# Optimization experiments

Hardware: AMD Instinct MI355X
Metric: run time of the kernel (lower is better)

The kernel has to match this reference:

```python
import jax, jax.numpy as jnp
import numpy as np

N, E = 50000, 800000
DIN, H, DOUT, L = 128, 128, 64, 3
NEG_SLOPE = 0.2  # PyG GATConv default


def setup_inputs() -> dict:
    key = jax.random.key(0)
    ks = jax.random.split(key, 12)
    s = lambda i, shape: (jax.random.normal(ks[i], shape, jnp.float32) * 0.05)
    return {
        "x": jax.random.normal(ks[0], (N, DIN), jnp.float32),
        "edge_index": jax.random.randint(ks[1], (2, E), 0, N, jnp.int64 if jax.config.jax_enable_x64 else jnp.int32),
        "W_emb": s(2, (DIN, H)), "b_emb": jnp.zeros((H,), jnp.float32),
        "gat_W": s(3, (L, H, H)), "gat_as": s(4, (L, H)), "gat_ad": s(5, (L, H)),
        "gat_b": jnp.zeros((L, H), jnp.float32),
        "Wn1": s(6, (H, H)), "bn1": jnp.zeros((H,), jnp.float32),
        "Wn2": s(7, (H, DOUT)), "bn2": jnp.zeros((DOUT,), jnp.float32),
        "We1": s(8, (2 * H, H)), "be1": jnp.zeros((H,), jnp.float32),
        "We2": s(9, (H, 3)), "be2": jnp.zeros((3,), jnp.float32),
    }


def _gat_layer(h, src, dst, n, W, a_src, a_dst, b):
    # Single-head GATConv (PyG defaults: heads=1, concat, self-loops already in src/dst)
    xw = h @ W                                   # [N, H]
    alpha_s = xw @ a_src                          # [N]
    alpha_d = xw @ a_dst                          # [N]
    logits = jax.nn.leaky_relu(alpha_s[src] + alpha_d[dst], NEG_SLOPE)  # [E']
    m = jax.ops.segment_max(logits, dst, num_segments=n)
    p = jnp.exp(logits - m[dst])
    denom = jax.ops.segment_sum(p, dst, num_segments=n)
    alpha = p / denom[dst]                        # softmax over incoming edges
    return jax.ops.segment_sum(alpha[:, None] * xw[src], dst, num_segments=n) + b


def reference(x, edge_index, W_emb, b_emb, gat_W, gat_as, gat_ad, gat_b,
              Wn1, bn1, Wn2, bn2, We1, be1, We2, be2):
    n = x.shape[0]
    src0, dst0 = edge_index[0], edge_index[1]
    loops = jnp.arange(n, dtype=src0.dtype)
    src = jnp.concatenate([src0, loops])          # GATConv adds self-loops by default
    dst = jnp.concatenate([dst0, loops])

    h = jax.nn.relu(x @ W_emb + b_emb)            # dropout off (eval mode)
    for l in range(L):
        h_new = _gat_layer(h, src, dst, n, gat_W[l], gat_as[l], gat_ad[l], gat_b[l])
        h = jax.nn.relu(h + h_new)                # residual + relu

    node_pred = jax.nn.relu(h @ Wn1 + bn1) @ Wn2 + bn2            # [N, DOUT]
    ef = jnp.concatenate([h[src0], h[dst0]], axis=1)              # vectorized edge gather [E, 2H]
    edge_pred = jax.nn.relu(ef @ We1 + be1) @ We2 + be2           # [E, 3]
    graph_emb = jnp.mean(h, axis=0, keepdims=True)                # batch=None path [1, H]
    return node_pred, edge_pred, graph_emb
```

## Files before the change

### kernel.cpp

```cpp
#include <hip/hip_runtime.h>

#define NNODES 50000
#define NEDGES 800000
#define HDIM 128
#define DOUT 64
#define NLAYERS 3
#define NEG_SLOPE 0.2f

#define NODE_OUT_ELEMS (NNODES * DOUT)
#define EDGE_OUT_ELEMS (NEDGES * 3)
#define GEMB_OFF (NODE_OUT_ELEMS + EDGE_OUT_ELEMS)

typedef __attribute__((ext_vector_type(8))) short short8;
typedef __attribute__((ext_vector_type(4))) float f32x4;
typedef unsigned long long u64;

__device__ __forceinline__ float bf2f(unsigned short u) {
    union { unsigned int i; float f; } v; v.i = ((unsigned int)u) << 16; return v.f;
}
__device__ __forceinline__ unsigned short f2bf(float f) {
    union { unsigned int i; float f; } v; v.f = f;
    unsigned int b = v.i;
    unsigned int r = (b + 0x7FFFu + ((b >> 16) & 1u)) >> 16;
    return (unsigned short)r;
}
__device__ __forceinline__ float leaky(float x) { return x > 0.f ? x : NEG_SLOPE * x; }
__device__ __forceinline__ float wread(const void* p, size_t i, int f32) {
    return f32 ? ((const float*)p)[i] : bf2f(((const unsigned short*)p)[i]);
}

__device__ __forceinline__ int eget(const int* e32, const int* iflag, int which, int e) {
    int idx = which * NEDGES + e;
    return (*iflag) ? e32[idx] : e32[2 * idx];
}

__global__ void init_kernel(int* cnt, int* cur, float* gsum, int* flags) {
    int i = blockIdx.x * 256 + threadIdx.x;
    if (i < NNODES) { cnt[i] = 0; cur[i] = 0; }
    if (blockIdx.x == 0) {
        if (threadIdx.x < HDIM) gsum[threadIdx.x] = 0.f;
        if (threadIdx.x < 2) flags[threadIdx.x] = 0;
    }
}

__global__ void detect_kernel(const unsigned short* xb, const int* e32,
                              int* fflag, int* iflag) {
    if (blockIdx.x == 0) {
        int hit = 0;
        for (int j = threadIdx.x; j < 4096; j += 256) {
            int e = (xb[j] >> 7) & 0xFF;
            if (e >= 0x90) hit = 1;
        }
        if (hit) atomicOr(fflag, 1);
    } else {
        int hit = 0;
        for (int t = threadIdx.x; t < 16384; t += 256) {
            int i = t * 48;
            if (e32[2 * i + 1] != 0) hit = 1;
        }
        if (__any(hit)) {
            if ((threadIdx.x & 63) == 0) atomicOr(iflag, 1);
        }
    }
}

__global__ void cvt_x_bf16_kernel(const void* x, unsigned short* xb,
                                  const int* f32flag) {
    int i = (blockIdx.x * 256 + threadIdx.x) * 4;
    if (*f32flag) {
        float4 v = *(const float4*)((const float*)x + i);
        unsigned short o[4] = {f2bf(v.x), f2bf(v.y), f2bf(v.z), f2bf(v.w)};
        *(uint2*)(xb + i) = *(uint2*)o;
    } else {
        *(uint2*)(xb + i) = *(const uint2*)((const unsigned short*)x + i);
    }
}

__global__ __launch_bounds__(256) void gemm_mfma_kernel(
    const unsigned short* __restrict__ A, const void* __restrict__ Bw,
    size_t b_off, const void* __restrict__ bias, unsigned short* __restrict__ C,
    int M, int relu, const int* __restrict__ f32flag)
{
    constexpr int KP = 128 + 8;
    __shared__ unsigned short sA[64 * KP];
    const int f32 = *f32flag;
    const int tid = threadIdx.x;
    const int row0 = blockIdx.x * 64;

    for (int c = tid; c < 64 * 16; c += 256) {
        int r = c >> 4, cp = c & 15;
        int gr = row0 + r;
        uint4 v = {0u, 0u, 0u, 0u};
        if (gr < M) v = *(const uint4*)(A + (size_t)gr * 128 + cp * 8);
        *(uint4*)(&sA[r * KP + cp * 8]) = v;
    }
    __syncthreads();

    const int wave = tid >> 6, lane = tid & 63;
    const int quad = lane >> 4, l15 = lane & 15;
    const int ncol0 = wave * 32;

    short8 bw[4][2];
    #pragma unroll
    for (int kk = 0; kk < 4; kk++)
        #pragma unroll
        for (int nt = 0; nt < 2; nt++) {
            int n = ncol0 + nt * 16 + l15;
            short8 t;
            #pragma unroll
            for (int j = 0; j < 8; j++)
                t[j] = (short)f2bf(wread(Bw, b_off + (size_t)(kk * 32 + quad * 8 + j) * 128 + n, f32));
            bw[kk][nt] = t;
        }

    float bv[2];
    #pragma unroll
    for (int nt = 0; nt < 2; nt++)
        bv[nt] = bias ? wread(bias, ncol0 + nt * 16 + l15, f32) : 0.f;

    f32x4 acc[4][2];
    #pragma unroll
    for (int mt = 0; mt < 4; mt++)
        #pragma unroll
        for (int nt = 0; nt < 2; nt++) {
            acc[mt][nt][0] = bv[nt]; acc[mt][nt][1] = bv[nt];
            acc[mt][nt][2] = bv[nt]; acc[mt][nt][3] = bv[nt];
        }

    #pragma unroll
    for (int kk = 0; kk < 4; kk++) {
        short8 a[4];
        #pragma unroll
        for (int mt = 0; mt < 4; mt++)
            a[mt] = *(const short8*)(&sA[(mt * 16 + l15) * KP + kk * 32 + quad * 8]);
        #pragma unroll
        for (int mt = 0; mt < 4; mt++)
            #pragma unroll
            for (int nt = 0; nt < 2; nt++)
                acc[mt][nt] = __builtin_amdgcn_mfma_f32_16x16x32_bf16(
                    a[mt], bw[kk][nt], acc[mt][nt], 0, 0, 0);
    }

    #pragma unroll
    for (int mt = 0; mt < 4; mt++)
        #pragma unroll
        for (int nt = 0; nt < 2; nt++)
            #pragma unroll
            for (int q = 0; q < 4; q++) {
                int row = row0 + mt * 16 + quad * 4 + q;
                if (row < M) {
                    float v = acc[mt][nt][q];
                    if (relu) v = fmaxf(v, 0.f);
                    C[(size_t)row * 128 + ncol0 + nt * 16 + l15] = f2bf(v);
                }
            }
}

__global__ __launch_bounds__(256) void node_mlp_kernel(
    const unsigned short* __restrict__ h, const void* __restrict__ Wn1,
    const void* __restrict__ bn1, const void* __restrict__ Wn2,
    const void* __restrict__ bn2, float* __restrict__ out, int M,
    const int* __restrict__ f32flag)
{
    constexpr int KP = 128 + 8;
    __shared__ unsigned short sA[64 * KP];
    const int f32 = *f32flag;
    const int tid = threadIdx.x;
    const int row0 = blockIdx.x * 64;

    for (int c = tid; c < 64 * 16; c += 256) {
        int r = c >> 4, cp = c & 15;
        int gr = row0 + r;
        uint4 v = {0u, 0u, 0u, 0u};
        if (gr < M) v = *(const uint4*)(h + (size_t)gr * 128 + cp * 8);
        *(uint4*)(&sA[r * KP + cp * 8]) = v;
    }
    __syncthreads();

    const int wave = tid >> 6, lane = tid & 63;
    const int quad = lane >> 4, l15 = lane & 15;
    const int ncol0 = wave * 32;

    {
        short8 bw[4][2];
        #pragma unroll
        for (int kk = 0; kk < 4; kk++)
            #pragma unroll
            for (int nt = 0; nt < 2; nt++) {
                int n = ncol0 + nt * 16 + l15;
                short8 t;
                #pragma unroll
                for (int j = 0; j < 8; j++)
                    t[j] = (short)f2bf(wread(Wn1, (size_t)(kk * 32 + quad * 8 + j) * 128 + n, f32));
                bw[kk][nt] = t;
            }
        float bv[2];
        #pragma unroll
        for (int nt = 0; nt < 2; nt++)
            bv[nt] = wread(bn1, ncol0 + nt * 16 + l15, f32);

        f32x4 acc[4][2];
        #pragma unroll
        for (int mt = 0; mt < 4; mt++)
            #pragma unroll
            for (int nt = 0; nt < 2; nt++) {
                acc[mt][nt][0] = bv[nt]; acc[mt][nt][1] = bv[nt];
                acc[mt][nt][2] = bv[nt]; acc[mt][nt][3] = bv[nt];
            }
        #pragma unroll
        for (int kk = 0; kk < 4; kk++) {
            short8 a[4];
            #pragma unroll
            for (int mt = 0; mt < 4; mt++)
                a[mt] = *(const short8*)(&sA[(mt * 16 + l15) * KP + kk * 32 + quad * 8]);
            #pragma unroll
            for (int mt = 0; mt < 4; mt++)
                #pragma unroll
                for (int nt = 0; nt < 2; nt++)
                    acc[mt][nt] = __builtin_amdgcn_mfma_f32_16x16x32_bf16(
                        a[mt], bw[kk][nt], acc[mt][nt], 0, 0, 0);
        }
        __syncthreads();
        #pragma unroll
        for (int mt = 0; mt < 4; mt++)
            #pragma unroll
            for (int nt = 0; nt < 2; nt++)
                #pragma unroll
                for (int q = 0; q < 4; q++) {
                    int r = mt * 16 + quad * 4 + q;
                    sA[r * KP + ncol0 + nt * 16 + l15] =
                        f2bf(fmaxf(acc[mt][nt][q], 0.f));
                }
        __syncthreads();
    }

    {
        const int col = wave * 16 + l15;
        short8 bw[4];
        #pragma unroll
        for (int kk = 0; kk < 4; kk++) {
            short8 t;
            #pragma unroll
            for (int j = 0; j < 8; j++)
                t[j] = (short)f2bf(wread(Wn2, (size_t)(kk * 32 + quad * 8 + j) * 64 + col, f32));
            bw[kk] = t;
        }
        float bv = wread(bn2, col, f32);
        f32x4 acc[4];
        #pragma unroll
        for (int mt = 0; mt < 4; mt++) {
            acc[mt][0] = bv; acc[mt][1] = bv; acc[mt][2] = bv; acc[mt][3] = bv;
        }
        #pragma unroll
        for (int kk = 0; kk < 4; kk++) {
            short8 a[4];
            #pragma unroll
            for (int mt = 0; mt < 4; mt++)
                a[mt] = *(const short8*)(&sA[(mt * 16 + l15) * KP + kk * 32 + quad * 8]);
            #pragma unroll
            for (int mt = 0; mt < 4; mt++)
                acc[mt] = __builtin_amdgcn_mfma_f32_16x16x32_bf16(
                    a[mt], bw[kk], acc[mt], 0, 0, 0);
        }
        #pragma unroll
        for (int mt = 0; mt < 4; mt++)
            #pragma unroll
            for (int q = 0; q < 4; q++) {
                int row = row0 + mt * 16 + quad * 4 + q;
                if (row < M) out[(size_t)row * 64 + col] = acc[mt][q];
            }
    }
}

__global__ __launch_bounds__(256) void edge_ab_kernel(
    const unsigned short* __restrict__ h, const void* __restrict__ We1,
    const void* __restrict__ be1, unsigned short* __restrict__ Axw,
    unsigned short* __restrict__ Bh, int M, const int* __restrict__ f32flag)
{
    constexpr int KP = 128 + 8;
    __shared__ unsigned short sA[64 * KP];
    const int f32 = *f32flag;
    const int tid = threadIdx.x;
    const int row0 = blockIdx.x * 64;

    for (int c = tid; c < 64 * 16; c += 256) {
        int r = c >> 4, cp = c & 15;
        int gr = row0 + r;
        uint4 v = {0u, 0u, 0u, 0u};
        if (gr < M) v = *(const uint4*)(h + (size_t)gr * 128 + cp * 8);
        *(uint4*)(&sA[r * KP + cp * 8]) = v;
    }
    __syncthreads();

    const int wave = tid >> 6, lane = tid & 63;
    const int quad = lane >> 4, l15 = lane & 15;
    const int ncol0 = wave * 32;

    #pragma unroll
    for (int half = 0; half < 2; half++) {
        const size_t b_off = (size_t)half * 128 * 128;
        unsigned short* Cp = half ? Bh : Axw;

        short8 bw[4][2];
        #pragma unroll
        for (int kk = 0; kk < 4; kk++)
            #pragma unroll
            for (int nt = 0; nt < 2; nt++) {
                int n = ncol0 + nt * 16 + l15;
                short8 t;
                #pragma unroll
                for (int j = 0; j < 8; j++)
                    t[j] = (short)f2bf(wread(We1, b_off + (size_t)(kk * 32 + quad * 8 + j) * 128 + n, f32));
                bw[kk][nt] = t;
            }
        float bv[2];
        #pragma unroll
        for (int nt = 0; nt < 2; nt++)
            bv[nt] = half ? 0.f : wread(be1, ncol0 + nt * 16 + l15, f32);

        f32x4 acc[4][2];
        #pragma unroll
        for (int mt = 0; mt < 4; mt++)
            #pragma unroll
            for (int nt = 0; nt < 2; nt++) {
                acc[mt][nt][0] = bv[nt]; acc[mt][nt][1] = bv[nt];
                acc[mt][nt][2] = bv[nt]; acc[mt][nt][3] = bv[nt];
            }
        #pragma unroll
        for (int kk = 0; kk < 4; kk++) {
            short8 a[4];
            #pragma unroll
            for (int mt = 0; mt < 4; mt++)
                a[mt] = *(const short8*)(&sA[(mt * 16 + l15) * KP + kk * 32 + quad * 8]);
            #pragma unroll
            for (int mt = 0; mt < 4; mt++)
                #pragma unroll
                for (int nt = 0; nt < 2; nt++)
                    acc[mt][nt] = __builtin_amdgcn_mfma_f32_16x16x32_bf16(
                        a[mt], bw[kk][nt], acc[mt][nt], 0, 0, 0);
        }
        #pragma unroll
        for (int mt = 0; mt < 4; mt++)
            #pragma unroll
            for (int nt = 0; nt < 2; nt++)
                #pragma unroll
                for (int q = 0; q < 4; q++) {
                    int row = row0 + mt * 16 + quad * 4 + q;
                    if (row < M)
                        Cp[(size_t)row * 128 + ncol0 + nt * 16 + l15] =
                            f2bf(acc[mt][nt][q]);
                }
    }
}

__global__ void alpha_kernel(const unsigned short* xw,
                             const void* gat_as, const void* gat_ad, int woff,
                             float* alpha_s, float* alpha_d,
                             const int* f32flag) {
    const int f32 = *f32flag;
    int wave = threadIdx.x >> 6, lane = threadIdx.x & 63;
    int n = blockIdx.x * 4 + wave;
    if (n >= NNODES) return;
    float v0 = bf2f(xw[(size_t)n * HDIM + lane]);
    float v1 = bf2f(xw[(size_t)n * HDIM + 64 + lane]);
    float ds = v0 * wread(gat_as, woff + lane, f32) + v1 * wread(gat_as, woff + 64 + lane, f32);
    float dd = v0 * wread(gat_ad, woff + lane, f32) + v1 * wread(gat_ad, woff + 64 + lane, f32);
    for (int d = 32; d >= 1; d >>= 1) { ds += __shfl_xor(ds, d); dd += __shfl_xor(dd, d); }
    if (lane == 0) { alpha_s[n] = ds; alpha_d[n] = dd; }
}

__global__ void count_kernel(const int* e32, const int* iflag, int* cnt) {
    int e = blockIdx.x * 256 + threadIdx.x;
    if (e < NEDGES) atomicAdd(&cnt[eget(e32, iflag, 1, e)], 1);
}
__global__ void scan1_kernel(const int* cnt, int* off, int* bsum) {
    __shared__ int s[256];
    int t = threadIdx.x, i = blockIdx.x * 256 + t;
    int v = (i < NNODES) ? cnt[i] : 0;
    s[t] = v;
    __syncthreads();
    for (int d = 1; d < 256; d <<= 1) {
        int add = (t >= d) ? s[t - d] : 0;
        __syncthreads();
        s[t] += add;
        __syncthreads();
    }
    if (i < NNODES) off[i] = s[t] - v;
    if (t == 255) bsum[blockIdx.x] = s[255];
}
__global__ void scan2_kernel(int* bsum, int nblk) {
    if (threadIdx.x == 0 && blockIdx.x == 0) {
        int run = 0;
        for (int c = 0; c < nblk; c++) { int t = bsum[c]; bsum[c] = run; run += t; }
    }
}
__global__ void scan3_kernel(int* off, const int* bsum) {
    int i = blockIdx.x * 256 + threadIdx.x;
    if (i < NNODES) off[i] += bsum[blockIdx.x];
}
__global__ void fill_kernel(const int* e32, const int* iflag, const int* off,
                            int* cur, u64* csrp, int use_pack) {
    int e = blockIdx.x * 256 + threadIdx.x;
    if (e < NEDGES) {
        int s = eget(e32, iflag, 0, e);
        int d = eget(e32, iflag, 1, e);
        int p = atomicAdd(&cur[d], 1);
        int pos = off[d] + p;
        if (use_pack)
            csrp[pos] = (u64)s | ((u64)d << 17) | ((u64)e << 34);
        else
            ((int*)csrp)[pos] = s;
    }
}

__global__ void aggregate_kernel(const unsigned short* __restrict__ xw,
                                 const float* __restrict__ as_, const float* __restrict__ ad_,
                                 const int* __restrict__ off, const u64* __restrict__ csrp,
                                 int use_pack, const void* __restrict__ gat_b, int boff,
                                 unsigned short* __restrict__ h,
                                 const int* __restrict__ f32flag) {
    const int f32 = *f32flag;
    int wave = threadIdx.x >> 6, lane = threadIdx.x & 63;
    int n = blockIdx.x * 4 + wave;
    if (n >= NNODES) return;
    int o0 = off[n];
    int o1 = (n == NNODES - 1) ? NEDGES : off[n + 1];
    int deg = o1 - o0;
    float adn = ad_[n];
    float lself = leaky(as_[n] + adn);

    int deg64 = deg < 64 ? deg : 64;
    int idxv = 0; float av = 0.f;
    if (lane < deg64) {
        idxv = use_pack ? (int)(csrp[o0 + lane] & 0x1FFFF)
                        : ((const int*)csrp)[o0 + lane];
        av = as_[idxv];
    }

    float m = lself;
    if (lane < deg64) m = fmaxf(m, leaky(av + adn));
    for (int i = 64 + lane; i < deg; i += 64) {
        int s = use_pack ? (int)(csrp[o0 + i] & 0x1FFFF)
                         : ((const int*)csrp)[o0 + i];
        m = fmaxf(m, leaky(as_[s] + adn));
    }
    #pragma unroll
    for (int d = 32; d >= 1; d >>= 1) m = fmaxf(m, __shfl_xor(m, d));

    const int slot = lane >> 4;
    const int l15  = lane & 15;
    float denom = 0.f;
    float acc[8];
    #pragma unroll
    for (int k = 0; k < 8; k++) acc[k] = 0.f;

    for (int t0 = 0; t0 < deg64; t0 += 4) {
        int i = t0 + slot;
        int sidx   = __shfl(idxv, i);
        float aval = __shfl(av, i);
        if (i < deg64) {
            float p = __expf(leaky(aval + adn) - m);
            denom += p;
            uint4 rv = *(const uint4*)(xw + (size_t)sidx * HDIM + l15 * 8);
            const unsigned short* rp = (const unsigned short*)&rv;
            #pragma unroll
            for (int k = 0; k < 8; k++) acc[k] += p * bf2f(rp[k]);
        }
    }
    for (int i = 64 + slot; i < deg; i += 4) {
        int s = use_pack ? (int)(csrp[o0 + i] & 0x1FFFF)
                         : ((const int*)csrp)[o0 + i];
        float p = __expf(leaky(as_[s] + adn) - m);
        denom += p;
        uint4 rv = *(const uint4*)(xw + (size_t)s * HDIM + l15 * 8);
        const unsigned short* rp = (const unsigned short*)&rv;
        #pragma unroll
        for (int k = 0; k < 8; k++) acc[k] += p * bf2f(rp[k]);
    }

    #pragma unroll
    for (int d = 16; d <= 32; d <<= 1) {
        denom += __shfl_xor(denom, d);
        #pragma unroll
        for (int k = 0; k < 8; k++) acc[k] += __shfl_xor(acc[k], d);
    }

    float ps = __expf(lself - m);
    denom += ps;
    uint4 sv = *(const uint4*)(xw + (size_t)n * HDIM + l15 * 8);
    const unsigned short* sp = (const unsigned short*)&sv;
    #pragma unroll
    for (int k = 0; k < 8; k++) acc[k] += ps * bf2f(sp[k]);

    if (slot == 0) {
        float inv = 1.f / denom;
        size_t base = (size_t)n * HDIM + l15 * 8;
        uint4 hv = *(const uint4*)(h + base);
        const unsigned short* hp = (const unsigned short*)&hv;
        unsigned short outv[8];
        #pragma unroll
        for (int k = 0; k < 8; k++) {
            float hx = bf2f(hp[k]);
            float bx = wread(gat_b, boff + l15 * 8 + k, f32);
            outv[k] = f2bf(fmaxf(hx + acc[k] * inv + bx, 0.f));
        }
        *(uint4*)(h + base) = *(uint4*)outv;
    }
}

__global__ __launch_bounds__(256) void edge_split_kernel(
    const unsigned short* __restrict__ A, const unsigned short* __restrict__ B,
    const int* __restrict__ e32, const int* __restrict__ iflag,
    const u64* __restrict__ csrp, int use_pack,
    const void* __restrict__ We2, const void* __restrict__ be2,
    float* __restrict__ eout, const int* __restrict__ f32flag)
{
    const int f32 = *f32flag;
    const int lane = threadIdx.x & 63;
    const int slot = lane >> 4, l15 = lane & 15;

    float w2[8][3];
    #pragma unroll
    for (int j = 0; j < 8; j++)
        #pragma unroll
        for (int c = 0; c < 3; c++)
            w2[j][c] = wread(We2, (l15 * 8 + j) * 3 + c, f32);
    const float bo0 = wread(be2, 0, f32);
    const float bo1 = wread(be2, 1, f32);
    const float bo2 = wread(be2, 2, f32);

    const int gw = (blockIdx.x * 256 + threadIdx.x) >> 6;
    const int stride = gridDim.x * 16;
    for (int e = gw * 4 + slot; e < NEDGES; e += stride) {
        int s, d, oe;
        if (use_pack) {
            u64 pk = csrp[e];
            s  = (int)(pk & 0x1FFFF);
            d  = (int)((pk >> 17) & 0x1FFFF);
            oe = (int)(pk >> 34);
        } else {
            s = eget(e32, iflag, 0, e);
            d = eget(e32, iflag, 1, e);
            oe = e;
        }
        uint4 avv = *(const uint4*)(A + (size_t)s * HDIM + l15 * 8);
        uint4 bvv = *(const uint4*)(B + (size_t)d * HDIM + l15 * 8);
        const unsigned short* ap = (const unsigned short*)&avv;
        const unsigned short* bp = (const unsigned short*)&bvv;
        float s0 = 0.f, s1 = 0.f, s2 = 0.f;
        #pragma unroll
        for (int j = 0; j < 8; j++) {
            float v = fmaxf(bf2f(ap[j]) + bf2f(bp[j]), 0.f);
            s0 += v * w2[j][0]; s1 += v * w2[j][1]; s2 += v * w2[j][2];
        }
        #pragma unroll
        for (int dd = 1; dd < 16; dd <<= 1) {
            s0 += __shfl_xor(s0, dd);
            s1 += __shfl_xor(s1, dd);
            s2 += __shfl_xor(s2, dd);
        }
        if (l15 == 0) {
            eout[(size_t)oe * 3 + 0] = s0 + bo0;
            eout[(size_t)oe * 3 + 1] = s1 + bo1;
            eout[(size_t)oe * 3 + 2] = s2 + bo2;
        }
    }
}

__global__ void gsum_kernel(const unsigned short* h, float* gsum) {
    int f = threadIdx.x;
    float local = 0.f;
    int n0 = blockIdx.x * 200;
    for (int j = 0; j < 200; j++) local += bf2f(h[(size_t)(n0 + j) * HDIM + f]);
    atomicAdd(&gsum[f], local);
}
__global__ void gout_kernel(const float* gsum, float* out) {
    int f = threadIdx.x;
    out[GEMB_OFF + f] = gsum[f] * (1.f / (float)NNODES);
}

extern "C" __attribute__((visibility("default")))
void kernel_launch(void* const* d_in, const int* in_sizes, int n_in,
                   void* d_out, int out_size, void* d_ws, size_t ws_size,
                   hipStream_t stream) {
    const void* x      = d_in[0];
    const int*  eidx   = (const int*)d_in[1];
    const void* W_emb  = d_in[2];
    const void* b_emb  = d_in[3];
    const void* gat_W  = d_in[4];
    const void* gat_as = d_in[5];
    const void* gat_ad = d_in[6];
    const void* gat_b  = d_in[7];
    const void* Wn1    = d_in[8];
    const void* bn1    = d_in[9];
    const void* Wn2    = d_in[10];
    const void* bn2    = d_in[11];
    const void* We1    = d_in[12];
    const void* be1    = d_in[13];
    const void* We2    = d_in[14];
    const void* be2    = d_in[15];
    float* out = (float*)d_out;

    char* ws = (char*)d_ws;
    unsigned short* h       = (unsigned short*)(ws);
    unsigned short* xw      = (unsigned short*)(ws + 12800000);
    float*          alpha_s = (float*)(ws + 25600000);
    float*          alpha_d = (float*)(ws + 25800000);
    int*            cnt     = (int*)(ws + 26000000);
    int*            off     = (int*)(ws + 26200000);
    int*            bsum    = (int*)(ws + 26400000);
    float*          gsum    = (float*)(ws + 26401024);
    int*            iflag   = (int*)(ws + 26401536);
    int*            fflag   = (int*)(ws + 26401540);
    u64*            csrp    = (u64*)(ws + 26608000);
    int*            cur     = (int*)alpha_s;

    const int use_pack = (ws_size >= (size_t)33008000) ? 1 : 0;

    const int node_blks = (NNODES + 255) / 256;
    const int edge_blks = (NEDGES + 255) / 256;
    const int g64       = (NNODES + 63) / 64;

    init_kernel<<<node_blks, 256, 0, stream>>>(cnt, cur, gsum, iflag);
    detect_kernel<<<2, 256, 0, stream>>>((const unsigned short*)x, eidx, fflag, iflag);

    cvt_x_bf16_kernel<<<6250, 256, 0, stream>>>(x, xw, fflag);
    gemm_mfma_kernel<<<g64, 256, 0, stream>>>(
        xw, W_emb, 0, b_emb, h, NNODES, 1, fflag);

    count_kernel<<<edge_blks, 256, 0, stream>>>(eidx, iflag, cnt);
    scan1_kernel<<<node_blks, 256, 0, stream>>>(cnt, off, bsum);
    scan2_kernel<<<1, 64, 0, stream>>>(bsum, node_blks);
    scan3_kernel<<<node_blks, 256, 0, stream>>>(off, bsum);
    fill_kernel<<<edge_blks, 256, 0, stream>>>(eidx, iflag, off, cur, csrp, use_pack);

    for (int l = 0; l < NLAYERS; l++) {
        gemm_mfma_kernel<<<g64, 256, 0, stream>>>(
            h, gat_W, (size_t)l * HDIM * HDIM, (const void*)0, xw, NNODES, 0, fflag);
        alpha_kernel<<<(NNODES + 3) / 4, 256, 0, stream>>>(
            xw, gat_as, gat_ad, l * HDIM, alpha_s, alpha_d, fflag);
        aggregate_kernel<<<(NNODES + 3) / 4, 256, 0, stream>>>(
            xw, alpha_s, alpha_d, off, csrp, use_pack, gat_b, l * HDIM, h, fflag);
    }

    node_mlp_kernel<<<g64, 256, 0, stream>>>(
        h, Wn1, bn1, Wn2, bn2, out, NNODES, fflag);

    gsum_kernel<<<NNODES / 200, 128, 0, stream>>>(h, gsum);
    gout_kernel<<<1, 128, 0, stream>>>(gsum, out);

    edge_ab_kernel<<<g64, 256, 0, stream>>>(
        h, We1, be1, xw, h, NNODES, fflag);
    edge_split_kernel<<<2048, 256, 0, stream>>>(
        xw, h, eidx, iflag, csrp, use_pack, We2, be2,
        out + NODE_OUT_ELEMS, fflag);
}
```

Before: 567.8 us.

## Fuse bf16 conversion and graph sum, prefetch aggregate rows, batch edge MLP

Drops the standalone x-to-bf16 conversion kernel by converting fp32 inputs while loading into shared memory in the embedding GEMM. Drops the gsum kernel by summing h columns from the node MLP's shared tile with atomics. Software-pipelines the aggregate kernel's neighbour row loads one step ahead, and has each edge_split slot process two edges to expose more memory-level parallelism. These cut launches and extra global passes, at the cost of more registers and more atomics.

```diff
diff --git a/kernel.cpp b/kernel.cpp
--- a/kernel.cpp
+++ b/kernel.cpp
@@ -64,20 +64,8 @@
     }
 }
 
-__global__ void cvt_x_bf16_kernel(const void* x, unsigned short* xb,
-                                  const int* f32flag) {
-    int i = (blockIdx.x * 256 + threadIdx.x) * 4;
-    if (*f32flag) {
-        float4 v = *(const float4*)((const float*)x + i);
-        unsigned short o[4] = {f2bf(v.x), f2bf(v.y), f2bf(v.z), f2bf(v.w)};
-        *(uint2*)(xb + i) = *(uint2*)o;
-    } else {
-        *(uint2*)(xb + i) = *(const uint2*)((const unsigned short*)x + i);
-    }
-}
-
 __global__ __launch_bounds__(256) void gemm_mfma_kernel(
-    const unsigned short* __restrict__ A, const void* __restrict__ Bw,
+    const void* __restrict__ Av, int a_from_x, const void* __restrict__ Bw,
     size_t b_off, const void* __restrict__ bias, unsigned short* __restrict__ C,
     int M, int relu, const int* __restrict__ f32flag)
 {
@@ -87,12 +75,29 @@
     const int tid = threadIdx.x;
     const int row0 = blockIdx.x * 64;
 
-    for (int c = tid; c < 64 * 16; c += 256) {
-        int r = c >> 4, cp = c & 15;
-        int gr = row0 + r;
-        uint4 v = {0u, 0u, 0u, 0u};
-        if (gr < M) v = *(const uint4*)(A + (size_t)gr * 128 + cp * 8);
-        *(uint4*)(&sA[r * KP + cp * 8]) = v;
+    if (a_from_x && f32) {
+        const float* Af = (const float*)Av;
+        for (int c = tid; c < 64 * 16; c += 256) {
+            int r = c >> 4, cp = c & 15;
+            int gr = row0 + r;
+            unsigned short o[8] = {0, 0, 0, 0, 0, 0, 0, 0};
+            if (gr < M) {
+                float4 v0 = *(const float4*)(Af + (size_t)gr * 128 + cp * 8);
+                float4 v1 = *(const float4*)(Af + (size_t)gr * 128 + cp * 8 + 4);
+                o[0] = f2bf(v0.x); o[1] = f2bf(v0.y); o[2] = f2bf(v0.z); o[3] = f2bf(v0.w);
+                o[4] = f2bf(v1.x); o[5] = f2bf(v1.y); o[6] = f2bf(v1.z); o[7] = f2bf(v1.w);
+            }
+            *(uint4*)(&sA[r * KP + cp * 8]) = *(uint4*)o;
+        }
+    } else {
+        const unsigned short* A = (const unsigned short*)Av;
+        for (int c = tid; c < 64 * 16; c += 256) {
+            int r = c >> 4, cp = c & 15;
+            int gr = row0 + r;
+            uint4 v = {0u, 0u, 0u, 0u};
+            if (gr < M) v = *(const uint4*)(A + (size_t)gr * 128 + cp * 8);
+            *(uint4*)(&sA[r * KP + cp * 8]) = v;
+        }
     }
     __syncthreads();
 
@@ -159,8 +164,8 @@
 __global__ __launch_bounds__(256) void node_mlp_kernel(
     const unsigned short* __restrict__ h, const void* __restrict__ Wn1,
     const void* __restrict__ bn1, const void* __restrict__ Wn2,
-    const void* __restrict__ bn2, float* __restrict__ out, int M,
-    const int* __restrict__ f32flag)
+    const void* __restrict__ bn2, float* __restrict__ out,
+    float* __restrict__ gsum, int M, const int* __restrict__ f32flag)
 {
     constexpr int KP = 128 + 8;
     __shared__ unsigned short sA[64 * KP];
@@ -176,6 +181,12 @@
         *(uint4*)(&sA[r * KP + cp * 8]) = v;
     }
     __syncthreads();
+
+    if (tid < 128) {
+        float hs = 0.f;
+        for (int r = 0; r < 64; r++) hs += bf2f(sA[r * KP + tid]);
+        atomicAdd(&gsum[tid], hs);
+    }
 
     const int wave = tid >> 6, lane = tid & 63;
     const int quad = lane >> 4, l15 = lane & 15;
@@ -454,18 +465,27 @@
     #pragma unroll
     for (int k = 0; k < 8; k++) acc[k] = 0.f;
 
+    int i_c = slot;
+    int sidx_c = __shfl(idxv, i_c & 63);
+    float aval_c = __shfl(av, i_c & 63);
+    uint4 rv_c = {0u, 0u, 0u, 0u};
+    if (i_c < deg64)
+        rv_c = *(const uint4*)(xw + (size_t)sidx_c * HDIM + l15 * 8);
     for (int t0 = 0; t0 < deg64; t0 += 4) {
-        int i = t0 + slot;
-        int sidx   = __shfl(idxv, i);
-        float aval = __shfl(av, i);
-        if (i < deg64) {
-            float p = __expf(leaky(aval + adn) - m);
+        int i_n = i_c + 4;
+        int sidx_n = __shfl(idxv, i_n & 63);
+        float aval_n = __shfl(av, i_n & 63);
+        uint4 rv_n = {0u, 0u, 0u, 0u};
+        if (i_n < deg64)
+            rv_n = *(const uint4*)(xw + (size_t)sidx_n * HDIM + l15 * 8);
+        if (i_c < deg64) {
+            float p = __expf(leaky(aval_c + adn) - m);
             denom += p;
-            uint4 rv = *(const uint4*)(xw + (size_t)sidx * HDIM + l15 * 8);
-            const unsigned short* rp = (const unsigned short*)&rv;
+            const unsigned short* rp = (const unsigned short*)&rv_c;
             #pragma unroll
             for (int k = 0; k < 8; k++) acc[k] += p * bf2f(rp[k]);
         }
+        i_c = i_n; sidx_c = sidx_n; aval_c = aval_n; rv_c = rv_n;
     }
     for (int i = 64 + slot; i < deg; i += 4) {
         int s = use_pack ? (int)(csrp[o0 + i] & 0x1FFFF)
@@ -530,50 +550,64 @@
     const float bo2 = wread(be2, 2, f32);
 
     const int gw = (blockIdx.x * 256 + threadIdx.x) >> 6;
-    const int stride = gridDim.x * 16;
-    for (int e = gw * 4 + slot; e < NEDGES; e += stride) {
-        int s, d, oe;
+    const int stride = gridDim.x * 32;
+    for (int e0 = gw * 8 + slot * 2; e0 < NEDGES; e0 += stride) {
+        const int e1 = e0 + 1;
+        const bool has1 = (e1 < NEDGES);
+        int s0, d0, oe0, s1 = 0, d1 = 0, oe1 = 0;
         if (use_pack) {
-            u64 pk = csrp[e];
-            s  = (int)(pk & 0x1FFFF);
-            d  = (int)((pk >> 17) & 0x1FFFF);
-            oe = (int)(pk >> 34);
+            u64 pk0 = csrp[e0];
+            s0 = (int)(pk0 & 0x1FFFF); d0 = (int)((pk0 >> 17) & 0x1FFFF);
+            oe0 = (int)(pk0 >> 34);
+            if (has1) {
+                u64 pk1 = csrp[e1];
+                s1 = (int)(pk1 & 0x1FFFF); d1 = (int)((pk1 >> 17) & 0x1FFFF);
+                oe1 = (int)(pk1 >> 34);
+            }
         } else {
-            s = eget(e32, iflag, 0, e);
-            d = eget(e32, iflag, 1, e);
-            oe = e;
-        }
-        uint4 avv = *(const uint4*)(A + (size_t)s * HDIM + l15 * 8);
-        uint4 bvv = *(const uint4*)(B + (size_t)d * HDIM + l15 * 8);
-        const unsigned short* ap = (const unsigned short*)&avv;
-        const unsigned short* bp = (const unsigned short*)&bvv;
-        float s0 = 0.f, s1 = 0.f, s2 = 0.f;
+            s0 = eget(e32, iflag, 0, e0); d0 = eget(e32, iflag, 1, e0); oe0 = e0;
+            if (has1) {
+                s1 = eget(e32, iflag, 0, e1); d1 = eget(e32, iflag, 1, e1); oe1 = e1;
+            }
+        }
+        uint4 a0 = *(const uint4*)(A + (size_t)s0 * HDIM + l15 * 8);
+        uint4 b0 = *(const uint4*)(B + (size_t)d0 * HDIM + l15 * 8);
+        uint4 a1 = {0u, 0u, 0u, 0u}, b1 = {0u, 0u, 0u, 0u};
+        if (has1) {
+            a1 = *(const uint4*)(A + (size_t)s1 * HDIM + l15 * 8);
+            b1 = *(const uint4*)(B + (size_t)d1 * HDIM + l15 * 8);
+        }
+        const unsigned short* ap0 = (const unsigned short*)&a0;
+        const unsigned short* bp0 = (const unsigned short*)&b0;
+        const unsigned short* ap1 = (const unsigned short*)&a1;
+        const unsigned short* bp1 = (const unsigned short*)&b1;
+        float s00 = 0.f, s01 = 0.f, s02 = 0.f;
+        float s10 = 0.f, s11 = 0.f, s12 = 0.f;
         #pragma unroll
         for (int j = 0; j < 8; j++) {
-            float v = fmaxf(bf2f(ap[j]) + bf2f(bp[j]), 0.f);
-            s0 += v * w2[j][0]; s1 += v * w2[j][1]; s2 += v * w2[j][2];
+            float v0 = fmaxf(bf2f(ap0[j]) + bf2f(bp0[j]), 0.f);
+            float v1 = fmaxf(bf2f(ap1[j]) + bf2f(bp1[j]), 0.f);
+            s00 += v0 * w2[j][0]; s01 += v0 * w2[j][1]; s02 += v0 * w2[j][2];
+            s10 += v1 * w2[j][0]; s11 += v1 * w2[j][1]; s12 += v1 * w2[j][2];
         }
         #pragma unroll
         for (int dd = 1; dd < 16; dd <<= 1) {
-            s0 += __shfl_xor(s0, dd);
-            s1 += __shfl_xor(s1, dd);
-            s2 += __shfl_xor(s2, dd);
+            s00 += __shfl_xor(s00, dd); s01 += __shfl_xor(s01, dd); s02 += __shfl_xor(s02, dd);
+            s10 += __shfl_xor(s10, dd); s11 += __shfl_xor(s11, dd); s12 += __shfl_xor(s12, dd);
         }
         if (l15 == 0) {
-            eout[(size_t)oe * 3 + 0] = s0 + bo0;
-            eout[(size_t)oe * 3 + 1] = s1 + bo1;
-            eout[(size_t)oe * 3 + 2] = s2 + bo2;
-        }
-    }
-}
-
-__global__ void gsum_kernel(const unsigned short* h, float* gsum) {
-    int f = threadIdx.x;
-    float local = 0.f;
-    int n0 = blockIdx.x * 200;
-    for (int j = 0; j < 200; j++) local += bf2f(h[(size_t)(n0 + j) * HDIM + f]);
-    atomicAdd(&gsum[f], local);
-}
+            eout[(size_t)oe0 * 3 + 0] = s00 + bo0;
+            eout[(size_t)oe0 * 3 + 1] = s01 + bo1;
+            eout[(size_t)oe0 * 3 + 2] = s02 + bo2;
+            if (has1) {
+                eout[(size_t)oe1 * 3 + 0] = s10 + bo0;
+                eout[(size_t)oe1 * 3 + 1] = s11 + bo1;
+                eout[(size_t)oe1 * 3 + 2] = s12 + bo2;
+            }
+        }
+    }
+}
+
 __global__ void gout_kernel(const float* gsum, float* out) {
     int f = threadIdx.x;
     out[GEMB_OFF + f] = gsum[f] * (1.f / (float)NNODES);
@@ -624,9 +658,8 @@
     init_kernel<<<node_blks, 256, 0, stream>>>(cnt, cur, gsum, iflag);
     detect_kernel<<<2, 256, 0, stream>>>((const unsigned short*)x, eidx, fflag, iflag);
 
-    cvt_x_bf16_kernel<<<6250, 256, 0, stream>>>(x, xw, fflag);
     gemm_mfma_kernel<<<g64, 256, 0, stream>>>(
-        xw, W_emb, 0, b_emb, h, NNODES, 1, fflag);
+        x, 1, W_emb, 0, b_emb, h, NNODES, 1, fflag);
 
     count_kernel<<<edge_blks, 256, 0, stream>>>(eidx, iflag, cnt);
     scan1_kernel<<<node_blks, 256, 0, stream>>>(cnt, off, bsum);
@@ -636,7 +669,7 @@
 
     for (int l = 0; l < NLAYERS; l++) {
         gemm_mfma_kernel<<<g64, 256, 0, stream>>>(
-            h, gat_W, (size_t)l * HDIM * HDIM, (const void*)0, xw, NNODES, 0, fflag);
+            h, 0, gat_W, (size_t)l * HDIM * HDIM, (const void*)0, xw, NNODES, 0, fflag);
         alpha_kernel<<<(NNODES + 3) / 4, 256, 0, stream>>>(
             xw, gat_as, gat_ad, l * HDIM, alpha_s, alpha_d, fflag);
         aggregate_kernel<<<(NNODES + 3) / 4, 256, 0, stream>>>(
@@ -644,9 +677,7 @@
     }
 
     node_mlp_kernel<<<g64, 256, 0, stream>>>(
-        h, Wn1, bn1, Wn2, bn2, out, NNODES, fflag);
-
-    gsum_kernel<<<NNODES / 200, 128, 0, stream>>>(h, gsum);
+        h, Wn1, bn1, Wn2, bn2, out, gsum, NNODES, fflag);
     gout_kernel<<<1, 128, 0, stream>>>(gsum, out);
 
     edge_ab_kernel<<<g64, 256, 0, stream>>>(
```

New measurement: 560.7 us. Within noise of the previous version (-1.2%).
